# Kernel optimization log

Measured on AMD Instinct MI355X. Metric: run time of the kernel, lower is better.

The kernel has to match this reference:

```python
import jax, jax.numpy as jnp
import numpy as np

HIDDEN = 2304
N_HEADS = 8
N_KV_HEADS = 4
HEAD_DIM = 256
SLIDING_WINDOW = 4096
QUERY_PRE_ATTN_SCALAR = 256.0
SOFTCAP = 50.0
ROPE_BASE = 10000.0


def setup_inputs() -> dict:
    key = jax.random.key(0)
    ks = jax.random.split(key, 6)
    B, S = 1, 4096
    scale = 0.02
    return {
        "hidden_states": jax.random.normal(ks[0], (B, S, HIDDEN), dtype=jnp.float32),
        "Wq": jax.random.normal(ks[1], (HIDDEN, N_HEADS * HEAD_DIM), dtype=jnp.float32) * scale,
        "Wk": jax.random.normal(ks[2], (HIDDEN, N_KV_HEADS * HEAD_DIM), dtype=jnp.float32) * scale,
        "Wv": jax.random.normal(ks[3], (HIDDEN, N_KV_HEADS * HEAD_DIM), dtype=jnp.float32) * scale,
        "Wo": jax.random.normal(ks[4], (N_HEADS * HEAD_DIM, HIDDEN), dtype=jnp.float32) * scale,
        "position_ids": jnp.arange(S, dtype=jnp.int64 if jax.config.jax_enable_x64 else jnp.int32)[None, :],
    }


def _rope_cos_sin(position_ids):
    # inv_freq: (head_dim//2,)
    inv_freq = 1.0 / (ROPE_BASE ** (jnp.arange(0, HEAD_DIM, 2, dtype=jnp.float32) / HEAD_DIM))
    freqs = position_ids.astype(jnp.float32)[..., None] * inv_freq[None, None, :]  # (B,S,hd/2)
    emb = jnp.concatenate([freqs, freqs], axis=-1)  # (B,S,hd)
    return jnp.cos(emb), jnp.sin(emb)


def _rotate_half(x):
    x1, x2 = jnp.split(x, 2, axis=-1)
    return jnp.concatenate([-x2, x1], axis=-1)


def reference(hidden_states, Wq, Wk, Wv, Wo, position_ids):
    B, S, _ = hidden_states.shape
    cos, sin = _rope_cos_sin(position_ids)  # (B,S,hd)
    cos = cos[:, None]  # (B,1,S,hd) broadcast over heads
    sin = sin[:, None]

    q = (hidden_states @ Wq).reshape(B, S, N_HEADS, HEAD_DIM).transpose(0, 2, 1, 3)
    k = (hidden_states @ Wk).reshape(B, S, N_KV_HEADS, HEAD_DIM).transpose(0, 2, 1, 3)
    v = (hidden_states @ Wv).reshape(B, S, N_KV_HEADS, HEAD_DIM).transpose(0, 2, 1, 3)

    q = q * cos + _rotate_half(q) * sin
    k = k * cos + _rotate_half(k) * sin

    # GQA: repeat kv heads to match query heads
    n_rep = N_HEADS // N_KV_HEADS
    k = jnp.repeat(k, n_rep, axis=1)  # (B,H,S,hd)
    v = jnp.repeat(v, n_rep, axis=1)

    scaling = QUERY_PRE_ATTN_SCALAR ** -0.5
    scores = jnp.einsum("bhqd,bhkd->bhqk", q, k) * scaling

    # attention logit softcapping
    scores = SOFTCAP * jnp.tanh(scores / SOFTCAP)

    # causal + sliding window mask
    qi = jnp.arange(S)[:, None]
    kj = jnp.arange(S)[None, :]
    mask = (kj <= qi) & (qi - kj < SLIDING_WINDOW)  # (S,S)
    scores = jnp.where(mask[None, None], scores, jnp.asarray(-1e30, scores.dtype))

    attn = jax.nn.softmax(scores, axis=-1)
    ctx = jnp.einsum("bhqk,bhkd->bhqd", attn, v)  # (B,H,S,hd)
    ctx = ctx.transpose(0, 2, 1, 3).reshape(B, S, N_HEADS * HEAD_DIM)
    return ctx @ Wo
```

## Files before the change

### kernel.cpp

```cpp
#include <hip/hip_runtime.h>
#include <cstdint>
#include <cstddef>

typedef unsigned short u16;
typedef short bf16x8 __attribute__((ext_vector_type(8)));
typedef float f32x4 __attribute__((ext_vector_type(4)));

#define S_LEN 4096
#define HID   2304
#define NH    8
#define NKV   4
#define HD    256
#define QD    2048
#define KD    1024
#define QKVW  4096
#define CHT   32
#define SLOTS_PER_HEAD 160

__device__ __forceinline__ u16 f2b(float f) {
    union { float f; uint32_t u; } v; v.f = f;
    uint32_t r = (v.u + 0x7FFFu + ((v.u >> 16) & 1u)) >> 16;
    return (u16)r;
}
__device__ __forceinline__ float b2f(u16 u) {
    union { uint32_t u; float f; } v; v.u = ((uint32_t)u) << 16;
    return v.f;
}

__device__ __forceinline__ void glds16(const void* g, void* l) {
    __builtin_amdgcn_global_load_lds(
        (__attribute__((address_space(1))) void*)(const_cast<void*>(g)),
        (__attribute__((address_space(3))) void*)l, 16, 0, 0);
}

__device__ __forceinline__ int slot_base(int qt) {
    int a = qt >> 4, b = qt & 15;
    return (a + 1) * (8 * a + b);
}

__device__ __forceinline__ float softcap_p(float s) {
    float u = s * 0.00125f;
    u = fminf(fmaxf(u, -0.53f), 0.53f);
    float u2 = u * u;
    float t50 = u * (50.0f + u2 * (-16.6666667f + 6.66666667f * u2));
    return __expf(t50);
}

__global__ __launch_bounds__(256) void cvt_h(const float* __restrict__ in, u16* __restrict__ out, int n4) {
    int id = blockIdx.x * 256 + threadIdx.x;
    if (id >= n4) return;
    float4 v = ((const float4*)in)[id];
    uint2 o;
    o.x = (uint32_t)f2b(v.x) | ((uint32_t)f2b(v.y) << 16);
    o.y = (uint32_t)f2b(v.z) | ((uint32_t)f2b(v.w) << 16);
    ((uint2*)out)[id] = o;
}

__device__ __forceinline__ void twcvt_body(const float* __restrict__ W, u16* __restrict__ out,
                                           int K, int N, int ldo, int n0, int k0) {
    __shared__ float T[64][68];
    const int t = threadIdx.x;
    for (int i = 0; i < 4; i++) {
        int id = i * 256 + t;
        int r = id >> 4, c4 = id & 15;
        float4 v = *(const float4*)(W + (size_t)(k0 + r) * N + n0 + c4 * 4);
        *(float4*)(&T[r][c4 * 4]) = v;
    }
    __syncthreads();
    for (int i = 0; i < 4; i++) {
        int id = i * 256 + t;
        int rn = id >> 4, c4 = id & 15;
        u16 a = f2b(T[c4 * 4 + 0][rn]);
        u16 b = f2b(T[c4 * 4 + 1][rn]);
        u16 c = f2b(T[c4 * 4 + 2][rn]);
        u16 d = f2b(T[c4 * 4 + 3][rn]);
        uint2 o;
        o.x = (uint32_t)a | ((uint32_t)b << 16);
        o.y = (uint32_t)c | ((uint32_t)d << 16);
        *(uint2*)(out + (size_t)(n0 + rn) * ldo + k0 + c4 * 4) = o;
    }
}

__global__ __launch_bounds__(256) void twcvt(const float* __restrict__ W, u16* __restrict__ out,
                                             int K, int N, int ldo) {
    twcvt_body(W, out, K, N, ldo, blockIdx.x * 64, blockIdx.y * 64);
}

__global__ __launch_bounds__(256) void twcvt_qkv(const float* __restrict__ Wq,
                                                 const float* __restrict__ Wk,
                                                 const float* __restrict__ Wv,
                                                 u16* __restrict__ out) {
    const int z = blockIdx.z;
    const float* W = (z == 0) ? Wq : (z == 1) ? Wk : Wv;
    const int N = (z == 0) ? QD : KD;
    const int n0 = blockIdx.x * 64;
    if (n0 >= N) return;
    u16* ob = out + ((z == 0) ? 0 : (z == 1) ? (size_t)QD * HID : (size_t)(QD + KD) * HID);
    twcvt_body(W, ob, HID, N, HID, n0, blockIdx.y * 64);
}

template<int BF16_OUT>
__global__ __launch_bounds__(512, 2) void gemm256(const u16* __restrict__ A, const u16* __restrict__ B,
                                                  void* __restrict__ Cp, int M, int N, int K) {
    const int tid = threadIdx.x;
    const int wv = tid >> 6, lane = tid & 63;
    const int quad = lane >> 4, m16 = lane & 15;
    const int gx = gridDim.x;
    int bid = blockIdx.y * gx + blockIdx.x;
    const int cpx = (gx * gridDim.y) >> 3;
    bid = (bid & 7) * cpx + (bid >> 3);
    const int m0 = (bid / gx) * 256, n0 = (bid % gx) * 256;
    const int wm = (wv & 1) * 128, wn = (wv >> 1) * 64;

    __shared__ __align__(16) u16 As[2][256 * 64];
    __shared__ __align__(16) u16 Bs[2][256 * 64];

    const int lr = lane >> 3, ls = lane & 7;
    const int scol = ((ls ^ lr) << 3);
    const u16* pA[4]; const u16* pB[4];
    int du[4];
#pragma unroll
    for (int j = 0; j < 4; j++) {
        int u = wv + 8 * j;
        pA[j] = A + (size_t)(m0 + u * 8 + lr) * K + scol;
        pB[j] = B + (size_t)(n0 + u * 8 + lr) * K + scol;
        du[j] = u * 512;
    }

    f32x4 acc[8][4];
#pragma unroll
    for (int i = 0; i < 8; i++)
#pragma unroll
        for (int j = 0; j < 4; j++) acc[i][j] = (f32x4){0.f, 0.f, 0.f, 0.f};

    const int aBase = (wm + m16) * 64;
    const int bBase = (wn + m16) * 64;
    const int s0 = ((quad ^ (m16 & 7)) << 3);
    const int s1 = s0 ^ 32;

    const int NT = K >> 6;
#pragma unroll
    for (int j = 0; j < 4; j++) glds16(pA[j], &As[0][du[j]]);
#pragma unroll
    for (int j = 0; j < 4; j++) glds16(pB[j], &Bs[0][du[j]]);
    asm volatile("s_waitcnt vmcnt(0)" ::: "memory");
    __builtin_amdgcn_sched_barrier(0);
    __builtin_amdgcn_s_barrier();

    for (int t = 0; t < NT; t++) {
        const int cur = t & 1, nxt = cur ^ 1;
        const int kn = (t + 1) << 6;
        const bool pre = (t + 1 < NT);
        bf16x8 af[4], bf[4];

#define MFMA16(IOFF)                                                               \
        _Pragma("unroll")                                                          \
        for (int i = 0; i < 4; i++)                                                \
            _Pragma("unroll")                                                      \
            for (int j = 0; j < 4; j++)                                            \
                acc[i + (IOFF)][j] =                                               \
                    __builtin_amdgcn_mfma_f32_16x16x32_bf16(af[i], bf[j],          \
                                                            acc[i + (IOFF)][j], 0, 0, 0);
#define PHASE_SYNC()                                                               \
        __builtin_amdgcn_s_barrier();                                              \
        asm volatile("s_waitcnt lgkmcnt(0)" ::: "memory");                         \
        __builtin_amdgcn_sched_barrier(0);

#pragma unroll
        for (int i = 0; i < 4; i++) af[i] = *(const bf16x8*)(&As[cur][aBase + i * 1024 + s0]);
#pragma unroll
        for (int j = 0; j < 4; j++) bf[j] = *(const bf16x8*)(&Bs[cur][bBase + j * 1024 + s0]);
        if (pre) {
#pragma unroll
            for (int j = 0; j < 4; j++) glds16(pA[j] + kn, &As[nxt][du[j]]);
        }
        PHASE_SYNC();
        __builtin_amdgcn_s_setprio(1);
        MFMA16(0);
        __builtin_amdgcn_s_setprio(0);
        __builtin_amdgcn_s_barrier();
#pragma unroll
        for (int i = 0; i < 4; i++) af[i] = *(const bf16x8*)(&As[cur][aBase + (i + 4) * 1024 + s0]);
        if (pre) {
#pragma unroll
            for (int j = 0; j < 4; j++) glds16(pB[j] + kn, &Bs[nxt][du[j]]);
        }
        PHASE_SYNC();
        __builtin_amdgcn_s_setprio(1);
        MFMA16(4);
        __builtin_amdgcn_s_setprio(0);
        __builtin_amdgcn_s_barrier();
#pragma unroll
        for (int i = 0; i < 4; i++) af[i] = *(const bf16x8*)(&As[cur][aBase + i * 1024 + s1]);
#pragma unroll
        for (int j = 0; j < 4; j++) bf[j] = *(const bf16x8*)(&Bs[cur][bBase + j * 1024 + s1]);
        PHASE_SYNC();
        __builtin_amdgcn_s_setprio(1);
        MFMA16(0);
        __builtin_amdgcn_s_setprio(0);
        __builtin_amdgcn_s_barrier();
#pragma unroll
        for (int i = 0; i < 4; i++) af[i] = *(const bf16x8*)(&As[cur][aBase + (i + 4) * 1024 + s1]);
        PHASE_SYNC();
        __builtin_amdgcn_s_setprio(1);
        MFMA16(4);
        __builtin_amdgcn_s_setprio(0);
        asm volatile("s_waitcnt vmcnt(0)" ::: "memory");
        __builtin_amdgcn_sched_barrier(0);
        __builtin_amdgcn_s_barrier();
#undef MFMA16
#undef PHASE_SYNC
    }
#pragma unroll
    for (int i = 0; i < 8; i++)
#pragma unroll
        for (int j = 0; j < 4; j++)
#pragma unroll
            for (int r = 0; r < 4; r++) {
                int row = m0 + wm + i * 16 + quad * 4 + r;
                int col = n0 + wn + j * 16 + m16;
                if (BF16_OUT) ((u16*)Cp)[(size_t)row * N + col] = f2b(acc[i][j][r]);
                else          ((float*)Cp)[(size_t)row * N + col] = acc[i][j][r];
            }
}

template<int BF16_OUT>
__global__ __launch_bounds__(256, 2) void gemm_bt(const u16* __restrict__ A, const u16* __restrict__ B,
                                                  void* __restrict__ Cp, int M, int N, int K) {
    const int tid  = threadIdx.x;
    const int wv = tid >> 6, lane = tid & 63;
    const int quad = lane >> 4, m16 = lane & 15;
    const int gx = gridDim.x;
    int bid = blockIdx.y * gx + blockIdx.x;
    const int cpx = (gx * gridDim.y) >> 3;
    bid = (bid & 7) * cpx + (bid >> 3);
    const int m0 = (bid / gx) * 128, n0 = (bid % gx) * 128;
    const int wm = (wv & 1) * 64, wn = (wv >> 1) * 64;
    __shared__ __align__(16) u16 As[128 * 32];
    __shared__ __align__(16) u16 Bs[128 * 32];
    int s0i = (wv * 2) * 64 + lane, s1i = s0i + 64;
    int row0 = s0i >> 2, c0 = (s0i & 3) ^ (row0 & 3);
    int row1 = s1i >> 2, c1 = (s1i & 3) ^ (row1 & 3);
    const u16* pA0 = A + (size_t)(m0 + row0) * K + c0 * 8;
    const u16* pA1 = A + (size_t)(m0 + row1) * K + c1 * 8;
    const u16* pB0 = B + (size_t)(n0 + row0) * K + c0 * 8;
    const u16* pB1 = B + (size_t)(n0 + row1) * K + c1 * 8;
    u16* lA0 = &As[(wv * 2 + 0) * 512]; u16* lA1 = &As[(wv * 2 + 1) * 512];
    u16* lB0 = &Bs[(wv * 2 + 0) * 512]; u16* lB1 = &Bs[(wv * 2 + 1) * 512];

    const f32x4 z4 = {0.f, 0.f, 0.f, 0.f};
    f32x4 acc00 = z4, acc01 = z4, acc02 = z4, acc03 = z4;
    f32x4 acc10 = z4, acc11 = z4, acc12 = z4, acc13 = z4;
    f32x4 acc20 = z4, acc21 = z4, acc22 = z4, acc23 = z4;
    f32x4 acc30 = z4, acc31 = z4, acc32 = z4, acc33 = z4;

    const int sw = quad ^ (m16 & 3);
    const u16* ra0 = &As[(wm + 0 * 16 + m16) * 32 + (sw << 3)];
    const u16* ra1 = &As[(wm + 1 * 16 + m16) * 32 + (sw << 3)];
    const u16* ra2 = &As[(wm + 2 * 16 + m16) * 32 + (sw << 3)];
    const u16* ra3 = &As[(wm + 3 * 16 + m16) * 32 + (sw << 3)];
    const u16* rb0 = &Bs[(wn + 0 * 16 + m16) * 32 + (sw << 3)];
    const u16* rb1 = &Bs[(wn + 1 * 16 + m16) * 32 + (sw << 3)];
    const u16* rb2 = &Bs[(wn + 2 * 16 + m16) * 32 + (sw << 3)];
    const u16* rb3 = &Bs[(wn + 3 * 16 + m16) * 32 + (sw << 3)];

    for (int k0 = 0; k0 < K; k0 += 32) {
        __syncthreads();
        glds16(pA0 + k0, lA0);
        glds16(pA1 + k0, lA1);
        glds16(pB0 + k0, lB0);
        glds16(pB1 + k0, lB1);
        __syncthreads();
        bf16x8 af0 = *(const bf16x8*)ra0, af1 = *(const bf16x8*)ra1;
        bf16x8 af2 = *(const bf16x8*)ra2, af3 = *(const bf16x8*)ra3;
        bf16x8 bf0 = *(const bf16x8*)rb0, bf1 = *(const bf16x8*)rb1;
        bf16x8 bf2 = *(const bf16x8*)rb2, bf3 = *(const bf16x8*)rb3;
        acc00 = __builtin_amdgcn_mfma_f32_16x16x32_bf16(af0, bf0, acc00, 0, 0, 0);
        acc01 = __builtin_amdgcn_mfma_f32_16x16x32_bf16(af0, bf1, acc01, 0, 0, 0);
        acc02 = __builtin_amdgcn_mfma_f32_16x16x32_bf16(af0, bf2, acc02, 0, 0, 0);
        acc03 = __builtin_amdgcn_mfma_f32_16x16x32_bf16(af0, bf3, acc03, 0, 0, 0);
        acc10 = __builtin_amdgcn_mfma_f32_16x16x32_bf16(af1, bf0, acc10, 0, 0, 0);
        acc11 = __builtin_amdgcn_mfma_f32_16x16x32_bf16(af1, bf1, acc11, 0, 0, 0);
        acc12 = __builtin_amdgcn_mfma_f32_16x16x32_bf16(af1, bf2, acc12, 0, 0, 0);
        acc13 = __builtin_amdgcn_mfma_f32_16x16x32_bf16(af1, bf3, acc13, 0, 0, 0);
        acc20 = __builtin_amdgcn_mfma_f32_16x16x32_bf16(af2, bf0, acc20, 0, 0, 0);
        acc21 = __builtin_amdgcn_mfma_f32_16x16x32_bf16(af2, bf1, acc21, 0, 0, 0);
        acc22 = __builtin_amdgcn_mfma_f32_16x16x32_bf16(af2, bf2, acc22, 0, 0, 0);
        acc23 = __builtin_amdgcn_mfma_f32_16x16x32_bf16(af2, bf3, acc23, 0, 0, 0);
        acc30 = __builtin_amdgcn_mfma_f32_16x16x32_bf16(af3, bf0, acc30, 0, 0, 0);
        acc31 = __builtin_amdgcn_mfma_f32_16x16x32_bf16(af3, bf1, acc31, 0, 0, 0);
        acc32 = __builtin_amdgcn_mfma_f32_16x16x32_bf16(af3, bf2, acc32, 0, 0, 0);
        acc33 = __builtin_amdgcn_mfma_f32_16x16x32_bf16(af3, bf3, acc33, 0, 0, 0);
    }

#define STORE_TILE(I, J, ACC)                                              \
    {                                                                      \
        _Pragma("unroll")                                                  \
        for (int r = 0; r < 4; r++) {                                      \
            int row = m0 + wm + (I) * 16 + quad * 4 + r;                   \
            int col = n0 + wn + (J) * 16 + m16;                            \
            float v = (ACC)[r];                                            \
            if (BF16_OUT) ((u16*)Cp)[(size_t)row * N + col] = f2b(v);      \
            else          ((float*)Cp)[(size_t)row * N + col] = v;         \
        }                                                                  \
    }
    STORE_TILE(0, 0, acc00) STORE_TILE(0, 1, acc01) STORE_TILE(0, 2, acc02) STORE_TILE(0, 3, acc03)
    STORE_TILE(1, 0, acc10) STORE_TILE(1, 1, acc11) STORE_TILE(1, 2, acc12) STORE_TILE(1, 3, acc13)
    STORE_TILE(2, 0, acc20) STORE_TILE(2, 1, acc21) STORE_TILE(2, 2, acc22) STORE_TILE(2, 3, acc23)
    STORE_TILE(3, 0, acc30) STORE_TILE(3, 1, acc31) STORE_TILE(3, 2, acc32) STORE_TILE(3, 3, acc33)
#undef STORE_TILE
}

__global__ __launch_bounds__(256) void rope_k(const u16* __restrict__ QKV, const int* __restrict__ pos,
                                              u16* __restrict__ Qb, u16* __restrict__ Kb) {
    int id = blockIdx.x * 256 + threadIdx.x;
    int s = id >> 7, j = id & 127;
    float p = (float)pos[s];
    float invf = expf(-0.07195578429985445f * (float)j);
    float ang = p * invf;
    float sn, cs;
    sincosf(ang, &sn, &cs);
    const u16* src = QKV + (size_t)s * QKVW;
    u16* dq = Qb + (size_t)s * QD;
#pragma unroll
    for (int h = 0; h < NH; h++) {
        float x1 = b2f(src[h * 256 + j]), x2 = b2f(src[h * 256 + 128 + j]);
        dq[h * 256 + j]       = f2b(x1 * cs - x2 * sn);
        dq[h * 256 + 128 + j] = f2b(x2 * cs + x1 * sn);
    }
    const u16* sk = src + QD;
    u16* dk = Kb + (size_t)s * KD;
#pragma unroll
    for (int h = 0; h < NKV; h++) {
        float x1 = b2f(sk[h * 256 + j]), x2 = b2f(sk[h * 256 + 128 + j]);
        dk[h * 256 + j]       = f2b(x1 * cs - x2 * sn);
        dk[h * 256 + 128 + j] = f2b(x2 * cs + x1 * sn);
    }
}

__global__ __launch_bounds__(256) void vtrans(const u16* __restrict__ QKV, u16* __restrict__ Vt) {
    const int s0 = blockIdx.x * 64, d0 = blockIdx.y * 64;
    __shared__ u16 T[64][72];
    const int t = threadIdx.x;
    for (int i = 0; i < 2; i++) {
        int id = i * 256 + t;
        int r = id >> 3, c = id & 7;
        uint4 v = *(const uint4*)(QKV + (size_t)(s0 + r) * QKVW + (QD + KD) + d0 + c * 8);
        *(uint4*)(&T[r][c * 8]) = v;
    }
    __syncthreads();
    for (int i = 0; i < 2; i++) {
        int id = i * 256 + t;
        int r = id >> 3, c = id & 7;
        union { u16 u[8]; uint4 v; } o;
        for (int jj = 0; jj < 8; jj++) o.u[jj] = T[c * 8 + jj][r];
        *(uint4*)(Vt + (size_t)(d0 + r) * S_LEN + s0 + c * 8) = o.v;
    }
}

__global__ __launch_bounds__(256, 3) void attn_part(const u16* __restrict__ Qb, const u16* __restrict__ Kb,
                                                    const u16* __restrict__ Vt,
                                                    u16* __restrict__ Part, float* __restrict__ Lpart) {
    const int tid  = threadIdx.x;
    const int wv = tid >> 6, lane = tid & 63;
    const int quad = lane >> 4, m16 = lane & 15;
    const int qt = blockIdx.x, h = blockIdx.y, ch = blockIdx.z;
    const int n_kvt = 2 * qt + 2;
    const int t0 = ch * CHT;
    if (t0 >= n_kvt) return;
    const int t1 = min(t0 + CHT, n_kvt);
    const int kvh = h >> 1;
    const int q0 = qt * 64;
    const int slot = h * SLOTS_PER_HEAD + slot_base(qt) + ch;

    __shared__ __align__(16) u16 Kl[2][32 * 256];
    __shared__ __align__(16) u16 Vl[256 * 32];
    __shared__ __align__(16) u16 Pl[4][16 * 32];

    int kOff[4], vOff[4];
#pragma unroll
    for (int i = 0; i < 4; i++) {
        int s = (wv * 4 + i) * 64 + lane;
        int kv = s >> 5, c = (s & 31) ^ (kv & 7);
        kOff[i] = kv * KD + c * 8;
        int d = s >> 2, cc = (s & 3) ^ ((d >> 1) & 3);
        vOff[i] = d * S_LEN + cc * 8;
    }
    const u16* Kbase = Kb + kvh * 256;
    const u16* Vbase = Vt + (size_t)(kvh * 256) * S_LEN;

    bf16x8 qf[8];
    {
        const u16* qp = Qb + (size_t)(q0 + wv * 16 + m16) * QD + h * 256 + quad * 8;
#pragma unroll
        for (int ks = 0; ks < 8; ks++) qf[ks] = *(const bf16x8*)(qp + ks * 32);
    }
    float li[4] = {0.f, 0.f, 0.f, 0.f};
    f32x4 o[4][4];
#pragma unroll
    for (int i = 0; i < 4; i++)
#pragma unroll
        for (int j = 0; j < 4; j++) o[i][j] = (f32x4){0.f, 0.f, 0.f, 0.f};

#pragma unroll
    for (int i = 0; i < 4; i++)
        glds16(Kbase + kOff[i] + t0 * (32 * KD), &Kl[0][(wv * 4 + i) * 512]);

    for (int kt = t0; kt < t1; kt++) {
        const int cur = (kt - t0) & 1, nxt = cur ^ 1;
        asm volatile("s_waitcnt vmcnt(0)" ::: "memory");
        __builtin_amdgcn_sched_barrier(0);
        __builtin_amdgcn_s_barrier();
#pragma unroll
        for (int i = 0; i < 4; i++)
            glds16(Vbase + vOff[i] + kt * 32, &Vl[(wv * 4 + i) * 512]);
        if (kt + 1 < t1) {
#pragma unroll
            for (int i = 0; i < 4; i++)
                glds16(Kbase + kOff[i] + (kt + 1) * (32 * KD), &Kl[nxt][(wv * 4 + i) * 512]);
        }
        f32x4 s[2];
        __builtin_amdgcn_s_setprio(1);
#pragma unroll
        for (int nt = 0; nt < 2; nt++) {
            f32x4 a = (f32x4){0.f, 0.f, 0.f, 0.f};
            int kr = nt * 16 + m16;
            int sw = kr & 7;
#pragma unroll
            for (int ks = 0; ks < 8; ks++) {
                int c = ks * 4 + quad;
                bf16x8 kf = *(const bf16x8*)(&Kl[cur][kr * 256 + ((c ^ sw) << 3)]);
                a = __builtin_amdgcn_mfma_f32_16x16x32_bf16(qf[ks], kf, a, 0, 0, 0);
            }
            s[nt] = a;
        }
        __builtin_amdgcn_s_setprio(0);
        const int kvb = kt * 32;
        u16* Pw = &Pl[wv][0];
        if (kvb + 31 <= q0) {
#pragma unroll
            for (int nt = 0; nt < 2; nt++)
#pragma unroll
                for (int r = 0; r < 4; r++) {
                    float p = softcap_p(s[nt][r]);
                    li[r] += p;
                    int m = quad * 4 + r;
                    int c = 2 * nt + (m16 >> 3);
                    int off = m16 & 7;
                    Pw[m * 32 + ((c ^ ((m >> 1) & 3)) << 3) + off] = f2b(p);
                }
        } else {
#pragma unroll
            for (int nt = 0; nt < 2; nt++)
#pragma unroll
                for (int r = 0; r < 4; r++) {
                    float p = softcap_p(s[nt][r]);
                    int kvg = kvb + nt * 16 + m16;
                    int qg  = q0 + wv * 16 + quad * 4 + r;
                    p = (kvg > qg) ? 0.f : p;
                    li[r] += p;
                    int m = quad * 4 + r;
                    int c = 2 * nt + (m16 >> 3);
                    int off = m16 & 7;
                    Pw[m * 32 + ((c ^ ((m >> 1) & 3)) << 3) + off] = f2b(p);
                }
        }
        if (kt + 1 < t1) {
            asm volatile("s_waitcnt vmcnt(4) lgkmcnt(0)" ::: "memory");
        } else {
            asm volatile("s_waitcnt vmcnt(0) lgkmcnt(0)" ::: "memory");
        }
        __builtin_amdgcn_sched_barrier(0);
        __builtin_amdgcn_s_barrier();
        bf16x8 pf[4];
#pragma unroll
        for (int qs = 0; qs < 4; qs++)
            pf[qs] = *(const bf16x8*)(&Pl[qs][m16 * 32 + ((quad ^ ((m16 >> 1) & 3)) << 3)]);
        __builtin_amdgcn_s_setprio(1);
#pragma unroll
        for (int dt = 0; dt < 4; dt++) {
            int d = wv * 64 + dt * 16 + m16;
            bf16x8 vf = *(const bf16x8*)(&Vl[d * 32 + ((quad ^ ((d >> 1) & 3)) << 3)]);
            o[0][dt] = __builtin_amdgcn_mfma_f32_16x16x32_bf16(pf[0], vf, o[0][dt], 0, 0, 0);
            o[1][dt] = __builtin_amdgcn_mfma_f32_16x16x32_bf16(pf[1], vf, o[1][dt], 0, 0, 0);
            o[2][dt] = __builtin_amdgcn_mfma_f32_16x16x32_bf16(pf[2], vf, o[2][dt], 0, 0, 0);
            o[3][dt] = __builtin_amdgcn_mfma_f32_16x16x32_bf16(pf[3], vf, o[3][dt], 0, 0, 0);
        }
        __builtin_amdgcn_s_setprio(0);
    }
    u16* Pp = Part + (size_t)slot * (64 * 256);
#pragma unroll
    for (int qs = 0; qs < 4; qs++)
#pragma unroll
        for (int dt = 0; dt < 4; dt++)
#pragma unroll
            for (int r = 0; r < 4; r++)
                Pp[(qs * 16 + quad * 4 + r) * 256 + wv * 64 + dt * 16 + m16] = f2b(o[qs][dt][r]);
#pragma unroll
    for (int r = 0; r < 4; r++) {
        float l = li[r];
        l += __shfl_xor(l, 1); l += __shfl_xor(l, 2);
        l += __shfl_xor(l, 4); l += __shfl_xor(l, 8);
        if (m16 == 0) Lpart[slot * 64 + wv * 16 + quad * 4 + r] = l;
    }
}

__global__ __launch_bounds__(256) void attn_combine(const u16* __restrict__ Part,
                                                    const float* __restrict__ Lpart,
                                                    u16* __restrict__ Ctx) {
    const int qt = blockIdx.x, h = blockIdx.y;
    const int nch = (qt >> 4) + 1;
    const int slot0 = h * SLOTS_PER_HEAD + slot_base(qt);
    const int t = threadIdx.x;
    const int q0 = qt * 64;
    __shared__ float linv[64];
    if (t < 64) {
        float l = 0.f;
        for (int c = 0; c < nch; c++) l += Lpart[(slot0 + c) * 64 + t];
        linv[t] = 1.f / l;
    }
    __syncthreads();
    const u16* P0 = Part + (size_t)slot0 * (64 * 256);
    for (int i = 0; i < 8; i++) {
        int idx = i * 256 + t;
        int row = idx >> 5, c8 = idx & 31;
        float acc[8] = {0.f,0.f,0.f,0.f,0.f,0.f,0.f,0.f};
        for (int c = 0; c < nch; c++) {
            uint4 v = *(const uint4*)(P0 + (size_t)c * (64 * 256) + row * 256 + c8 * 8);
            uint32_t w[4] = {v.x, v.y, v.z, v.w};
            for (int k = 0; k < 4; k++) {
                acc[k * 2]     += b2f((u16)(w[k] & 0xFFFF));
                acc[k * 2 + 1] += b2f((u16)(w[k] >> 16));
            }
        }
        float iv = linv[row];
        uint4 ov;
        uint32_t* op = (uint32_t*)&ov;
        for (int k = 0; k < 4; k++)
            op[k] = (uint32_t)f2b(acc[k * 2] * iv) | ((uint32_t)f2b(acc[k * 2 + 1] * iv) << 16);
        *(uint4*)(Ctx + (size_t)(q0 + row) * QD + h * 256 + c8 * 8) = ov;
    }
}

extern "C" void kernel_launch(void* const* d_in, const int* in_sizes, int n_in,
                              void* d_out, int out_size, void* d_ws, size_t ws_size,
                              hipStream_t stream) {
    const float* H  = (const float*)d_in[0];
    const float* Wq = (const float*)d_in[1];
    const float* Wk = (const float*)d_in[2];
    const float* Wv = (const float*)d_in[3];
    const float* Wo = (const float*)d_in[4];
    const int* pos  = (const int*)d_in[5];
    float* out = (float*)d_out;

    char* ws = (char*)d_ws;
    size_t off = 0;
    u16* Hb     = (u16*)(ws + off); off += (size_t)S_LEN * HID * 2;
    u16* Wqkvt  = (u16*)(ws + off); off += (size_t)QKVW * HID * 2;
    u16* Wot    = (u16*)(ws + off); off += (size_t)HID * QD * 2;
    u16* QKVraw = (u16*)(ws + off); off += (size_t)S_LEN * QKVW * 2;
    u16* Qb     = (u16*)(ws + off); off += (size_t)S_LEN * QD * 2;
    u16* Kb     = (u16*)(ws + off); off += (size_t)S_LEN * KD * 2;
    u16* Vt     = (u16*)(ws + off); off += (size_t)KD * S_LEN * 2;
    u16* Ctx    = (u16*)(ws + off); off += (size_t)S_LEN * QD * 2;
    u16* Part   = (u16*)(ws + off);  off += (size_t)NH * SLOTS_PER_HEAD * 64 * 256 * 2;
    float* Lprt = (float*)(ws + off); off += (size_t)NH * SLOTS_PER_HEAD * 64 * 4;

    cvt_h<<<dim3((S_LEN * HID / 4 + 255) / 256), dim3(256), 0, stream>>>(H, Hb, S_LEN * HID / 4);
    twcvt_qkv<<<dim3(32, HID / 64, 3), dim3(256), 0, stream>>>(Wq, Wk, Wv, Wqkvt);
    twcvt<<<dim3(HID / 64, QD / 64), dim3(256), 0, stream>>>(Wo, Wot, QD, HID, QD);
    gemm256<1><<<dim3(QKVW / 256, S_LEN / 256), dim3(512), 0, stream>>>(Hb, Wqkvt, QKVraw, S_LEN, QKVW, HID);
    rope_k<<<dim3(S_LEN * 128 / 256), dim3(256), 0, stream>>>(QKVraw, pos, Qb, Kb);
    vtrans<<<dim3(S_LEN / 64, KD / 64), dim3(256), 0, stream>>>(QKVraw, Vt);
    attn_part<<<dim3(64, NH, 4), dim3(256), 0, stream>>>(Qb, Kb, Vt, Part, Lprt);
    attn_combine<<<dim3(64, NH), dim3(256), 0, stream>>>(Part, Lprt, Ctx);
    gemm_bt<0><<<dim3(HID / 128, S_LEN / 128), dim3(256), 0, stream>>>(Ctx, Wot, out, S_LEN, HID, QD);
}
```

Measured before the change: 428.4 us.

## Merge prep and rope/vtrans launches, schedule heaviest attention tiles first

Combines the three input/weight conversion kernels into one launch and the RoPE and V-transpose kernels into another, dispatching work by block index range. The attention partial and combine kernels now use a flattened grid that issues the longest causal query tiles first (qt descending, heads interleaved). The aim is fewer launch gaps and tail imbalance. In exchange there is some branch divergence between block roles and the shared-memory tile is allocated for every block in the fused kernels.

```diff
diff --git a/kernel.cpp b/kernel.cpp
--- a/kernel.cpp
+++ b/kernel.cpp
@@ -46,19 +46,8 @@
     return __expf(t50);
 }
 
-__global__ __launch_bounds__(256) void cvt_h(const float* __restrict__ in, u16* __restrict__ out, int n4) {
-    int id = blockIdx.x * 256 + threadIdx.x;
-    if (id >= n4) return;
-    float4 v = ((const float4*)in)[id];
-    uint2 o;
-    o.x = (uint32_t)f2b(v.x) | ((uint32_t)f2b(v.y) << 16);
-    o.y = (uint32_t)f2b(v.z) | ((uint32_t)f2b(v.w) << 16);
-    ((uint2*)out)[id] = o;
-}
-
 __device__ __forceinline__ void twcvt_body(const float* __restrict__ W, u16* __restrict__ out,
-                                           int K, int N, int ldo, int n0, int k0) {
-    __shared__ float T[64][68];
+                                           int K, int N, int ldo, int n0, int k0, float (*T)[68]) {
     const int t = threadIdx.x;
     for (int i = 0; i < 4; i++) {
         int id = i * 256 + t;
@@ -81,22 +70,40 @@
     }
 }
 
-__global__ __launch_bounds__(256) void twcvt(const float* __restrict__ W, u16* __restrict__ out,
-                                             int K, int N, int ldo) {
-    twcvt_body(W, out, K, N, ldo, blockIdx.x * 64, blockIdx.y * 64);
-}
-
-__global__ __launch_bounds__(256) void twcvt_qkv(const float* __restrict__ Wq,
-                                                 const float* __restrict__ Wk,
-                                                 const float* __restrict__ Wv,
-                                                 u16* __restrict__ out) {
-    const int z = blockIdx.z;
-    const float* W = (z == 0) ? Wq : (z == 1) ? Wk : Wv;
-    const int N = (z == 0) ? QD : KD;
-    const int n0 = blockIdx.x * 64;
-    if (n0 >= N) return;
-    u16* ob = out + ((z == 0) ? 0 : (z == 1) ? (size_t)QD * HID : (size_t)(QD + KD) * HID);
-    twcvt_body(W, ob, HID, N, HID, n0, blockIdx.y * 64);
+#define PREP_CVT   9216
+#define PREP_QKV   3456
+#define PREP_WO    1152
+__global__ __launch_bounds__(256) void prep_all(const float* __restrict__ H,
+                                                const float* __restrict__ Wq,
+                                                const float* __restrict__ Wk,
+                                                const float* __restrict__ Wv,
+                                                const float* __restrict__ Wo,
+                                                u16* __restrict__ Hb,
+                                                u16* __restrict__ Wqkvt,
+                                                u16* __restrict__ Wot) {
+    __shared__ float T[64][68];
+    const int bid = blockIdx.x;
+    if (bid < PREP_CVT) {
+        int id = bid * 256 + threadIdx.x;
+        float4 v = ((const float4*)H)[id];
+        uint2 o;
+        o.x = (uint32_t)f2b(v.x) | ((uint32_t)f2b(v.y) << 16);
+        o.y = (uint32_t)f2b(v.z) | ((uint32_t)f2b(v.w) << 16);
+        ((uint2*)Hb)[id] = o;
+    } else if (bid < PREP_CVT + PREP_QKV) {
+        int b = bid - PREP_CVT;
+        int bx = b & 31; int rest = b >> 5; int by = rest % 36; int z = rest / 36;
+        const float* W = (z == 0) ? Wq : (z == 1) ? Wk : Wv;
+        const int N = (z == 0) ? QD : KD;
+        const int n0 = bx * 64;
+        if (n0 >= N) return;
+        u16* ob = Wqkvt + ((z == 0) ? 0 : (z == 1) ? (size_t)QD * HID : (size_t)(QD + KD) * HID);
+        twcvt_body(W, ob, HID, N, HID, n0, by * 64, T);
+    } else {
+        int b = bid - PREP_CVT - PREP_QKV;
+        int bx = b % 36, by = b / 36;
+        twcvt_body(Wo, Wot, QD, HID, QD, bx * 64, by * 64, T);
+    }
 }
 
 template<int BF16_OUT>
@@ -311,50 +318,54 @@
 #undef STORE_TILE
 }
 
-__global__ __launch_bounds__(256) void rope_k(const u16* __restrict__ QKV, const int* __restrict__ pos,
-                                              u16* __restrict__ Qb, u16* __restrict__ Kb) {
-    int id = blockIdx.x * 256 + threadIdx.x;
-    int s = id >> 7, j = id & 127;
-    float p = (float)pos[s];
-    float invf = expf(-0.07195578429985445f * (float)j);
-    float ang = p * invf;
-    float sn, cs;
-    sincosf(ang, &sn, &cs);
-    const u16* src = QKV + (size_t)s * QKVW;
-    u16* dq = Qb + (size_t)s * QD;
-#pragma unroll
-    for (int h = 0; h < NH; h++) {
-        float x1 = b2f(src[h * 256 + j]), x2 = b2f(src[h * 256 + 128 + j]);
-        dq[h * 256 + j]       = f2b(x1 * cs - x2 * sn);
-        dq[h * 256 + 128 + j] = f2b(x2 * cs + x1 * sn);
-    }
-    const u16* sk = src + QD;
-    u16* dk = Kb + (size_t)s * KD;
-#pragma unroll
-    for (int h = 0; h < NKV; h++) {
-        float x1 = b2f(sk[h * 256 + j]), x2 = b2f(sk[h * 256 + 128 + j]);
-        dk[h * 256 + j]       = f2b(x1 * cs - x2 * sn);
-        dk[h * 256 + 128 + j] = f2b(x2 * cs + x1 * sn);
-    }
-}
-
-__global__ __launch_bounds__(256) void vtrans(const u16* __restrict__ QKV, u16* __restrict__ Vt) {
-    const int s0 = blockIdx.x * 64, d0 = blockIdx.y * 64;
-    __shared__ u16 T[64][72];
-    const int t = threadIdx.x;
-    for (int i = 0; i < 2; i++) {
-        int id = i * 256 + t;
-        int r = id >> 3, c = id & 7;
-        uint4 v = *(const uint4*)(QKV + (size_t)(s0 + r) * QKVW + (QD + KD) + d0 + c * 8);
-        *(uint4*)(&T[r][c * 8]) = v;
-    }
-    __syncthreads();
-    for (int i = 0; i < 2; i++) {
-        int id = i * 256 + t;
-        int r = id >> 3, c = id & 7;
-        union { u16 u[8]; uint4 v; } o;
-        for (int jj = 0; jj < 8; jj++) o.u[jj] = T[c * 8 + jj][r];
-        *(uint4*)(Vt + (size_t)(d0 + r) * S_LEN + s0 + c * 8) = o.v;
+#define RV_ROPE 2048
+__global__ __launch_bounds__(256) void rope_vtrans(const u16* __restrict__ QKV, const int* __restrict__ pos,
+                                                   u16* __restrict__ Qb, u16* __restrict__ Kb,
+                                                   u16* __restrict__ Vt) {
+    const int bid = blockIdx.x;
+    if (bid < RV_ROPE) {
+        int id = bid * 256 + threadIdx.x;
+        int s = id >> 7, j = id & 127;
+        float p = (float)pos[s];
+        float invf = expf(-0.07195578429985445f * (float)j);
+        float ang = p * invf;
+        float sn, cs;
+        sincosf(ang, &sn, &cs);
+        const u16* src = QKV + (size_t)s * QKVW;
+        u16* dq = Qb + (size_t)s * QD;
+#pragma unroll
+        for (int h = 0; h < NH; h++) {
+            float x1 = b2f(src[h * 256 + j]), x2 = b2f(src[h * 256 + 128 + j]);
+            dq[h * 256 + j]       = f2b(x1 * cs - x2 * sn);
+            dq[h * 256 + 128 + j] = f2b(x2 * cs + x1 * sn);
+        }
+        const u16* sk = src + QD;
+        u16* dk = Kb + (size_t)s * KD;
+#pragma unroll
+        for (int h = 0; h < NKV; h++) {
+            float x1 = b2f(sk[h * 256 + j]), x2 = b2f(sk[h * 256 + 128 + j]);
+            dk[h * 256 + j]       = f2b(x1 * cs - x2 * sn);
+            dk[h * 256 + 128 + j] = f2b(x2 * cs + x1 * sn);
+        }
+    } else {
+        __shared__ u16 T[64][72];
+        int vb = bid - RV_ROPE;
+        const int s0 = (vb & 63) * 64, d0 = (vb >> 6) * 64;
+        const int t = threadIdx.x;
+        for (int i = 0; i < 2; i++) {
+            int id = i * 256 + t;
+            int r = id >> 3, c = id & 7;
+            uint4 v = *(const uint4*)(QKV + (size_t)(s0 + r) * QKVW + (QD + KD) + d0 + c * 8);
+            *(uint4*)(&T[r][c * 8]) = v;
+        }
+        __syncthreads();
+        for (int i = 0; i < 2; i++) {
+            int id = i * 256 + t;
+            int r = id >> 3, c = id & 7;
+            union { u16 u[8]; uint4 v; } o;
+            for (int jj = 0; jj < 8; jj++) o.u[jj] = T[c * 8 + jj][r];
+            *(uint4*)(Vt + (size_t)(d0 + r) * S_LEN + s0 + c * 8) = o.v;
+        }
     }
 }
 
@@ -364,7 +375,11 @@
     const int tid  = threadIdx.x;
     const int wv = tid >> 6, lane = tid & 63;
     const int quad = lane >> 4, m16 = lane & 15;
-    const int qt = blockIdx.x, h = blockIdx.y, ch = blockIdx.z;
+    const int bid = blockIdx.x;
+    const int xc = bid >> 3;
+    const int h  = bid & 7;
+    const int qt = 63 - (xc >> 2);
+    const int ch = xc & 3;
     const int n_kvt = 2 * qt + 2;
     const int t0 = ch * CHT;
     if (t0 >= n_kvt) return;
@@ -508,7 +523,8 @@
 __global__ __launch_bounds__(256) void attn_combine(const u16* __restrict__ Part,
                                                     const float* __restrict__ Lpart,
                                                     u16* __restrict__ Ctx) {
-    const int qt = blockIdx.x, h = blockIdx.y;
+    const int qt = 63 - blockIdx.x;
+    const int h = blockIdx.y;
     const int nch = (qt >> 4) + 1;
     const int slot0 = h * SLOTS_PER_HEAD + slot_base(qt);
     const int t = threadIdx.x;
@@ -566,13 +582,10 @@
     u16* Part   = (u16*)(ws + off);  off += (size_t)NH * SLOTS_PER_HEAD * 64 * 256 * 2;
     float* Lprt = (float*)(ws + off); off += (size_t)NH * SLOTS_PER_HEAD * 64 * 4;
 
-    cvt_h<<<dim3((S_LEN * HID / 4 + 255) / 256), dim3(256), 0, stream>>>(H, Hb, S_LEN * HID / 4);
-    twcvt_qkv<<<dim3(32, HID / 64, 3), dim3(256), 0, stream>>>(Wq, Wk, Wv, Wqkvt);
-    twcvt<<<dim3(HID / 64, QD / 64), dim3(256), 0, stream>>>(Wo, Wot, QD, HID, QD);
+    prep_all<<<dim3(PREP_CVT + PREP_QKV + PREP_WO), dim3(256), 0, stream>>>(H, Wq, Wk, Wv, Wo, Hb, Wqkvt, Wot);
     gemm256<1><<<dim3(QKVW / 256, S_LEN / 256), dim3(512), 0, stream>>>(Hb, Wqkvt, QKVraw, S_LEN, QKVW, HID);
-    rope_k<<<dim3(S_LEN * 128 / 256), dim3(256), 0, stream>>>(QKVraw, pos, Qb, Kb);
-    vtrans<<<dim3(S_LEN / 64, KD / 64), dim3(256), 0, stream>>>(QKVraw, Vt);
-    attn_part<<<dim3(64, NH, 4), dim3(256), 0, stream>>>(Qb, Kb, Vt, Part, Lprt);
+    rope_vtrans<<<dim3(RV_ROPE + 1024), dim3(256), 0, stream>>>(QKVraw, pos, Qb, Kb, Vt);
+    attn_part<<<dim3(2048), dim3(256), 0, stream>>>(Qb, Kb, Vt, Part, Lprt);
     attn_combine<<<dim3(64, NH), dim3(256), 0, stream>>>(Part, Lprt, Ctx);
     gemm_bt<0><<<dim3(HID / 128, S_LEN / 128), dim3(256), 0, stream>>>(Ctx, Wot, out, S_LEN, HID, QD);
 }
```

After: 459.6 us. 7.3% more time.
